# Kernel tuning notes

Measured on AMD Instinct MI355X. Metric: run time of the kernel, lower is better.

Reference implementation:

```python
import jax, jax.numpy as jnp
import numpy as np
from jax import lax

B, N, T, H, E, D, K = 2, 1024, 4096, 256, 2, 2, 9


def angle2vector(a):
    return jnp.stack([jnp.sin(a), jnp.cos(a)], axis=-1)


def setup_inputs() -> dict:
    key = jax.random.key(0)
    ks = jax.random.split(key, 16)
    s = jnp.float32(0.05)
    return {
        "x": jax.random.normal(ks[0], (B, N, T), jnp.float32),
        "z": jax.random.uniform(ks[1], (B, T, E, D), jnp.float32, 0.0, 2.0 * np.pi),
        # encoder: depthwise conv (groups=N) then two 1x1 convs
        "dw_w": jax.random.normal(ks[2], (N, 1, K), jnp.float32) * s,
        "dw_b": jax.random.normal(ks[3], (N,), jnp.float32) * s,
        "w1": jax.random.normal(ks[4], (H, N), jnp.float32) * s,
        "b1": jax.random.normal(ks[5], (H,), jnp.float32) * s,
        "w2": jax.random.normal(ks[6], (H, H), jnp.float32) * s,
        "b2": jax.random.normal(ks[7], (H,), jnp.float32) * s,
        # heads (1x1 convs)
        "wm": jax.random.normal(ks[8], (E * D * 2, H), jnp.float32) * s,
        "bm": jax.random.normal(ks[9], (E * D * 2,), jnp.float32) * s,
        "wv": jax.random.normal(ks[10], (E * D, H), jnp.float32) * s,
        "bv": jax.random.normal(ks[11], (E * D,), jnp.float32) * s,
        # feature basis / readout params
        "receptive_fields": jax.random.uniform(ks[12], (N, E, D), jnp.float32, 0.0, 2.0 * np.pi),
        "ensemble_weights": jax.random.normal(ks[13], (N, E), jnp.float32),
        "final_scale": jax.random.normal(ks[14], (N,), jnp.float32) * s,
        "log_tuning_width": jnp.full((1,), np.log(2.0), jnp.float32),
    }


def reference(x, z, dw_w, dw_b, w1, b1, w2, b2, wm, bm, wv, bv,
              receptive_fields, ensemble_weights, final_scale, log_tuning_width):
    # ---- encoder ----
    # depthwise conv1d, kernel_size=K, padding='same', groups=N
    h = lax.conv_general_dilated(
        x, dw_w, window_strides=(1,), padding="SAME",
        feature_group_count=N, dimension_numbers=("NCH", "OIH", "NCH"))
    h = h + dw_b[None, :, None]
    h = jax.nn.relu(jnp.einsum("hn,bnt->bht", w1, h) + b1[None, :, None])
    h = jax.nn.relu(jnp.einsum("gh,bht->bgt", w2, h) + b2[None, :, None])

    # ---- heads ----
    mu = jnp.einsum("oh,bht->bot", wm, h) + bm[None, :, None]  # [B, E*D*2, T]
    mu = mu.transpose(0, 2, 1).reshape(B, T, E, D, 2)
    logvar = jnp.einsum("oh,bht->bot", wv, h) + bv[None, :, None]  # [B, E*D, T]
    logvar = logvar.transpose(0, 2, 1).reshape(B, T, E, D)
    # normalize encodings onto unit circle
    mu = mu / jnp.sqrt(jnp.sum(mu ** 2, axis=-1, keepdims=True))

    # ---- feature basis ('bump') ----
    zv = angle2vector(z)                     # [B, T, E, D, 2]
    rfv = angle2vector(receptive_fields)     # [N, E, D, 2]
    diff = zv[:, :, None] - rfv[None, None]  # [B, T, N, E, D, 2]
    dist = jnp.sum(diff ** 2, axis=(4, 5))   # [B, T, N, E]
    response = jnp.exp(-dist / jnp.exp(log_tuning_width))  # nonlinearity='exp'

    # ---- ensemble-weighted readout ----
    ew = jax.nn.softmax(ensemble_weights, axis=1)  # [N, E]
    responses = jnp.einsum("btne,ne->btn", response, ew)
    responses = responses * jnp.exp(final_scale)[None, None]
    responses = responses.transpose(0, 2, 1)  # [B, N, T]
    return responses, z, mu, logvar
```

## Files before the change

kernel.cpp:

```cpp
#include <hip/hip_runtime.h>
#include <hip/hip_bf16.h>

#define B_ 2
#define N_ 1024
#define T_ 4096
#define H_ 256
#define ROWS_ 8192

typedef float f32x4 __attribute__((ext_vector_type(4)));
typedef __bf16 bf16x8 __attribute__((ext_vector_type(8)));

__device__ __forceinline__ void gl16(const void* g, void* l) {
  __builtin_amdgcn_global_load_lds(
      (const __attribute__((address_space(1))) void*)g,
      (__attribute__((address_space(3))) void*)l, 16, 0, 0);
}

__global__ __launch_bounds__(256) void cvt_split(
    const float* __restrict__ w1, const float* __restrict__ w2,
    __bf16* __restrict__ w1h, __bf16* __restrict__ w1l,
    __bf16* __restrict__ w2h, __bf16* __restrict__ w2l) {
  int i = blockIdx.x * 256 + threadIdx.x;
  if (i < 262144) {
    float v = w1[i];
    __bf16 h = (__bf16)v;
    w1h[i] = h;
    w1l[i] = (__bf16)(v - (float)h);
  } else {
    int j = i - 262144;
    float v = w2[j];
    __bf16 h = (__bf16)v;
    w2h[j] = h;
    w2l[j] = (__bf16)(v - (float)h);
  }
}

__global__ __launch_bounds__(256) void dwconv_t(
    const float* __restrict__ x, const float* __restrict__ w,
    const float* __restrict__ bias, __bf16* __restrict__ h0h,
    __bf16* __restrict__ h0l) {
  __shared__ float xs[64][73];
  const int tid = threadIdx.x;
  const int t0 = blockIdx.x * 64;
  const int n0 = blockIdx.y * 64;
  const int b = blockIdx.z;
  for (int i = tid; i < 64 * 72; i += 256) {
    int rr = i / 72, cc = i % 72;
    int tt = t0 - 4 + cc;
    xs[rr][cc] = (tt >= 0 && tt < T_) ? x[((size_t)(b * N_ + n0 + rr)) * T_ + tt] : 0.f;
  }
  __syncthreads();
  const int nl = tid & 63;
  const int tg = tid >> 6;
  float wr[9];
  #pragma unroll
  for (int k = 0; k < 9; ++k) wr[k] = w[(n0 + nl) * 9 + k];
  const float bb = bias[n0 + nl];
  for (int j = 0; j < 16; ++j) {
    int tl = tg * 16 + j;
    float acc = bb;
    #pragma unroll
    for (int k = 0; k < 9; ++k) acc = fmaf(xs[nl][tl + k], wr[k], acc);
    size_t o = ((size_t)b * T_ + t0 + tl) * N_ + n0 + nl;
    __bf16 h = (__bf16)acc;
    h0h[o] = h;
    h0l[o] = (__bf16)(acc - (float)h);
  }
}

__global__ __launch_bounds__(256) void gemm3p(
    const __bf16* __restrict__ Ah, const __bf16* __restrict__ Al,
    const __bf16* __restrict__ Wh, const __bf16* __restrict__ Wl,
    const float* __restrict__ bias, __bf16* __restrict__ Oh,
    __bf16* __restrict__ Ol, int K, int relu) {
  __shared__ __bf16 As[2][2][128 * 32];
  __shared__ __bf16 Ws[2][2][64 * 32];
  const int tid = threadIdx.x;
  int orig = blockIdx.y * 4 + blockIdx.x;
  int rm = (orig & 7) * 32 + (orig >> 3);
  const int g0 = (rm & 3) * 64;
  const int row0 = (rm >> 2) * 128;

  const int sr = tid >> 2;
  const int sl = tid & 3;
  const size_t a_off0 = (size_t)(row0 + sr) * K + sl * 8;
  const size_t a_off1 = (size_t)(row0 + 64 + sr) * K + sl * 8;
  const size_t w_off = (size_t)(g0 + sr) * K + sl * 8;

  const int lane = tid & 63;
  const int wid = tid >> 6;
  const int wrr = (wid >> 1) * 64;
  const int wcc = (wid & 1) * 32;
  const int lr = lane & 15;
  const int ls = lane >> 4;

  f32x4 acc[4][2];
  #pragma unroll
  for (int i = 0; i < 4; ++i)
    #pragma unroll
    for (int j = 0; j < 2; ++j) acc[i][j] = (f32x4)0.f;

  auto STAGE = [&](int buf, int k0) {
    gl16(Ah + a_off0 + k0, &As[buf][0][tid * 8]);
    gl16(Ah + a_off1 + k0, &As[buf][0][(tid + 256) * 8]);
    gl16(Al + a_off0 + k0, &As[buf][1][tid * 8]);
    gl16(Al + a_off1 + k0, &As[buf][1][(tid + 256) * 8]);
    gl16(Wh + w_off + k0, &Ws[buf][0][tid * 8]);
    gl16(Wl + w_off + k0, &Ws[buf][1][tid * 8]);
  };

  const int nk = K >> 5;
  STAGE(0, 0);
  __syncthreads();
  for (int kt = 0; kt < nk; ++kt) {
    const int cur = kt & 1;
    if (kt + 1 < nk) STAGE(cur ^ 1, (kt + 1) << 5);
    bf16x8 ah[4], al[4], wh[2], wl[2];
    #pragma unroll
    for (int mi = 0; mi < 4; ++mi) {
      int r = wrr + mi * 16 + lr;
      ah[mi] = *(const bf16x8*)&As[cur][0][r * 32 + ls * 8];
      al[mi] = *(const bf16x8*)&As[cur][1][r * 32 + ls * 8];
    }
    #pragma unroll
    for (int ni = 0; ni < 2; ++ni) {
      int r = wcc + ni * 16 + lr;
      wh[ni] = *(const bf16x8*)&Ws[cur][0][r * 32 + ls * 8];
      wl[ni] = *(const bf16x8*)&Ws[cur][1][r * 32 + ls * 8];
    }
    #pragma unroll
    for (int mi = 0; mi < 4; ++mi)
      #pragma unroll
      for (int ni = 0; ni < 2; ++ni) {
        acc[mi][ni] = __builtin_amdgcn_mfma_f32_16x16x32_bf16(ah[mi], wh[ni], acc[mi][ni], 0, 0, 0);
        acc[mi][ni] = __builtin_amdgcn_mfma_f32_16x16x32_bf16(ah[mi], wl[ni], acc[mi][ni], 0, 0, 0);
        acc[mi][ni] = __builtin_amdgcn_mfma_f32_16x16x32_bf16(al[mi], wh[ni], acc[mi][ni], 0, 0, 0);
      }
    __syncthreads();
  }

  #pragma unroll
  for (int ni = 0; ni < 2; ++ni) {
    const int g = g0 + wcc + ni * 16 + lr;
    const float bb = bias[g];
    #pragma unroll
    for (int mi = 0; mi < 4; ++mi)
      #pragma unroll
      for (int reg = 0; reg < 4; ++reg) {
        int t = row0 + wrr + mi * 16 + ls * 4 + reg;
        float v = acc[mi][ni][reg] + bb;
        if (relu) v = fmaxf(v, 0.f);
        __bf16 h = (__bf16)v;
        Oh[(size_t)t * H_ + g] = h;
        Ol[(size_t)t * H_ + g] = (__bf16)(v - (float)h);
      }
  }
}

__global__ __launch_bounds__(256) void heads_t(
    const __bf16* __restrict__ h2h, const __bf16* __restrict__ h2l,
    const float* __restrict__ wm, const float* __restrict__ bm,
    const float* __restrict__ wv, const float* __restrict__ bv,
    float* __restrict__ out_mu, float* __restrict__ out_lv) {
  __shared__ float sw[12][256];
  const int tid = threadIdx.x;
  for (int i = tid; i < 8 * 256; i += 256) sw[i >> 8][i & 255] = wm[i];
  for (int i = tid; i < 4 * 256; i += 256) sw[8 + (i >> 8)][i & 255] = wv[i];
  __syncthreads();
  const int tq = tid & 3;
  const int tl = tid >> 2;
  const size_t row = blockIdx.x * 64 + tl;
  float s[12];
  #pragma unroll
  for (int o = 0; o < 12; ++o) s[o] = 0.f;
  for (int j = 0; j < 8; ++j) {
    int jj = (j + tq * 2) & 7;
    int k0 = tq * 64 + jj * 8;
    bf16x8 vh = *(const bf16x8*)&h2h[row * 256 + k0];
    bf16x8 vl = *(const bf16x8*)&h2l[row * 256 + k0];
    #pragma unroll
    for (int e = 0; e < 8; ++e) {
      float v = (float)vh[e] + (float)vl[e];
      #pragma unroll
      for (int o = 0; o < 12; ++o) s[o] = fmaf(sw[o][k0 + e], v, s[o]);
    }
  }
  #pragma unroll
  for (int o = 0; o < 12; ++o) {
    s[o] += __shfl_xor(s[o], 1);
    s[o] += __shfl_xor(s[o], 2);
  }
  if (tq == 0) {
    float4 m01, m23;
    float mm[8];
    #pragma unroll
    for (int ed = 0; ed < 4; ++ed) {
      float m0 = s[ed * 2] + bm[ed * 2];
      float m1 = s[ed * 2 + 1] + bm[ed * 2 + 1];
      float inv = 1.f / sqrtf(m0 * m0 + m1 * m1);
      mm[ed * 2] = m0 * inv;
      mm[ed * 2 + 1] = m1 * inv;
    }
    m01 = make_float4(mm[0], mm[1], mm[2], mm[3]);
    m23 = make_float4(mm[4], mm[5], mm[6], mm[7]);
    *(float4*)&out_mu[row * 8] = m01;
    *(float4*)&out_mu[row * 8 + 4] = m23;
  } else if (tq == 1) {
    float4 lv = make_float4(s[8] + bv[0], s[9] + bv[1], s[10] + bv[2], s[11] + bv[3]);
    *(float4*)&out_lv[row * 4] = lv;
  }
}

__global__ __launch_bounds__(256) void resp_kernel(
    const float* __restrict__ z, const float* __restrict__ rf,
    const float* __restrict__ ew, const float* __restrict__ fs,
    const float* __restrict__ ltw, float* __restrict__ out,
    float* __restrict__ out_z) {
  __shared__ float s_sin[64][4];
  __shared__ float s_cos[64][4];
  __shared__ float s_w[64][2];
  const int tid = threadIdx.x;
  const int tc = blockIdx.x;
  const int nc = blockIdx.y;
  const int b = blockIdx.z;
  {
    int nl = tid >> 2, ed = tid & 3;
    float a = rf[(nc * 64 + nl) * 4 + ed];
    s_sin[nl][ed] = sinf(a);
    s_cos[nl][ed] = cosf(a);
  }
  if (tid < 64) {
    int n = nc * 64 + tid;
    float e0 = ew[n * 2], e1 = ew[n * 2 + 1];
    float m = fmaxf(e0, e1);
    float x0 = expf(e0 - m), x1 = expf(e1 - m);
    float sc = expf(fs[n]) / (x0 + x1);
    s_w[tid][0] = x0 * sc;
    s_w[tid][1] = x1 * sc;
  }
  __syncthreads();
  const int t = tc * 256 + tid;
  const float inv_tw = expf(-ltw[0]);
  float4 zv = *(const float4*)&z[((size_t)b * T_ + t) * 4];
  if (nc == 0) *(float4*)&out_z[((size_t)b * T_ + t) * 4] = zv;
  float sz0 = sinf(zv.x), cz0 = cosf(zv.x);
  float sz1 = sinf(zv.y), cz1 = cosf(zv.y);
  float sz2 = sinf(zv.z), cz2 = cosf(zv.z);
  float sz3 = sinf(zv.w), cz3 = cosf(zv.w);
  float* op = out + (size_t)b * N_ * T_ + (size_t)(nc * 64) * T_ + t;
  #pragma unroll 4
  for (int nl = 0; nl < 64; ++nl) {
    float dot0 = sz0 * s_sin[nl][0] + cz0 * s_cos[nl][0] +
                 sz1 * s_sin[nl][1] + cz1 * s_cos[nl][1];
    float dot1 = sz2 * s_sin[nl][2] + cz2 * s_cos[nl][2] +
                 sz3 * s_sin[nl][3] + cz3 * s_cos[nl][3];
    float r0 = __expf((2.f * dot0 - 4.f) * inv_tw);
    float r1 = __expf((2.f * dot1 - 4.f) * inv_tw);
    op[(size_t)nl * T_] = s_w[nl][0] * r0 + s_w[nl][1] * r1;
  }
}

extern "C" void kernel_launch(void* const* d_in, const int* in_sizes, int n_in,
                              void* d_out, int out_size, void* d_ws, size_t ws_size,
                              hipStream_t stream) {
  const float* x   = (const float*)d_in[0];
  const float* z   = (const float*)d_in[1];
  const float* dww = (const float*)d_in[2];
  const float* dwb = (const float*)d_in[3];
  const float* w1  = (const float*)d_in[4];
  const float* b1  = (const float*)d_in[5];
  const float* w2  = (const float*)d_in[6];
  const float* b2  = (const float*)d_in[7];
  const float* wm  = (const float*)d_in[8];
  const float* bm  = (const float*)d_in[9];
  const float* wv  = (const float*)d_in[10];
  const float* bv  = (const float*)d_in[11];
  const float* rf  = (const float*)d_in[12];
  const float* ew  = (const float*)d_in[13];
  const float* fs  = (const float*)d_in[14];
  const float* ltw = (const float*)d_in[15];

  float* out = (float*)d_out;
  float* out_resp = out;
  float* out_z    = out + (size_t)B_ * N_ * T_;
  float* out_mu   = out_z + (size_t)B_ * T_ * 4;
  float* out_lv   = out_mu + (size_t)B_ * T_ * 8;

  __bf16* h0h = (__bf16*)out_resp;
  __bf16* h0l = h0h + (size_t)ROWS_ * N_;

  __bf16* p = (__bf16*)d_ws;
  __bf16* w1h = p; p += 262144;
  __bf16* w1l = p; p += 262144;
  __bf16* w2h = p; p += 65536;
  __bf16* w2l = p; p += 65536;
  __bf16* h1h = p; p += (size_t)ROWS_ * H_;
  __bf16* h1l = p; p += (size_t)ROWS_ * H_;
  __bf16* h2h = p; p += (size_t)ROWS_ * H_;
  __bf16* h2l = p; p += (size_t)ROWS_ * H_;

  cvt_split<<<1280, 256, 0, stream>>>(w1, w2, w1h, w1l, w2h, w2l);
  dwconv_t<<<dim3(T_ / 64, N_ / 64, B_), 256, 0, stream>>>(x, dww, dwb, h0h, h0l);
  gemm3p<<<dim3(4, ROWS_ / 128, 1), 256, 0, stream>>>(
      h0h, h0l, w1h, w1l, b1, h1h, h1l, N_, 1);
  gemm3p<<<dim3(4, ROWS_ / 128, 1), 256, 0, stream>>>(
      h1h, h1l, w2h, w2l, b2, h2h, h2l, H_, 1);
  heads_t<<<dim3(ROWS_ / 64), 256, 0, stream>>>(
      h2h, h2l, wm, bm, wv, bv, out_mu, out_lv);
  resp_kernel<<<dim3(T_ / 256, N_ / 64, B_), 256, 0, stream>>>(
      z, rf, ew, fs, ltw, out_resp, out_z);
}
```

Before: 197.3 us.

## Shrink GEMM row tile to 64, swizzle LDS, and register-window the dwconv

```diff
diff --git a/kernel.cpp b/kernel.cpp
--- a/kernel.cpp
+++ b/kernel.cpp
@@ -39,7 +39,7 @@
     const float* __restrict__ x, const float* __restrict__ w,
     const float* __restrict__ bias, __bf16* __restrict__ h0h,
     __bf16* __restrict__ h0l) {
-  __shared__ float xs[64][73];
+  __shared__ float xs[64][76];
   const int tid = threadIdx.x;
   const int t0 = blockIdx.x * 64;
   const int n0 = blockIdx.y * 64;
@@ -49,22 +49,26 @@
     int tt = t0 - 4 + cc;
     xs[rr][cc] = (tt >= 0 && tt < T_) ? x[((size_t)(b * N_ + n0 + rr)) * T_ + tt] : 0.f;
   }
-  __syncthreads();
   const int nl = tid & 63;
   const int tg = tid >> 6;
   float wr[9];
   #pragma unroll
   for (int k = 0; k < 9; ++k) wr[k] = w[(n0 + nl) * 9 + k];
   const float bb = bias[n0 + nl];
+  __syncthreads();
+  float win[24];
+  #pragma unroll
+  for (int c = 0; c < 6; ++c)
+    *(f32x4*)&win[c * 4] = *(const f32x4*)&xs[nl][tg * 16 + c * 4];
+  const size_t obase = ((size_t)b * T_ + t0 + tg * 16) * N_ + n0 + nl;
+  #pragma unroll
   for (int j = 0; j < 16; ++j) {
-    int tl = tg * 16 + j;
     float acc = bb;
     #pragma unroll
-    for (int k = 0; k < 9; ++k) acc = fmaf(xs[nl][tl + k], wr[k], acc);
-    size_t o = ((size_t)b * T_ + t0 + tl) * N_ + n0 + nl;
+    for (int k = 0; k < 9; ++k) acc = fmaf(win[j + k], wr[k], acc);
     __bf16 h = (__bf16)acc;
-    h0h[o] = h;
-    h0l[o] = (__bf16)(acc - (float)h);
+    h0h[obase + (size_t)j * N_] = h;
+    h0l[obase + (size_t)j * N_] = (__bf16)(acc - (float)h);
   }
 }
 
@@ -73,41 +77,41 @@
     const __bf16* __restrict__ Wh, const __bf16* __restrict__ Wl,
     const float* __restrict__ bias, __bf16* __restrict__ Oh,
     __bf16* __restrict__ Ol, int K, int relu) {
-  __shared__ __bf16 As[2][2][128 * 32];
+  __shared__ __bf16 As[2][2][64 * 32];
   __shared__ __bf16 Ws[2][2][64 * 32];
   const int tid = threadIdx.x;
-  int orig = blockIdx.y * 4 + blockIdx.x;
-  int rm = (orig & 7) * 32 + (orig >> 3);
+  const int orig = blockIdx.x;
+  const int rm = (orig & 7) * 64 + (orig >> 3);
   const int g0 = (rm & 3) * 64;
-  const int row0 = (rm >> 2) * 128;
+  const int row0 = (rm >> 2) * 64;
 
   const int sr = tid >> 2;
   const int sl = tid & 3;
-  const size_t a_off0 = (size_t)(row0 + sr) * K + sl * 8;
-  const size_t a_off1 = (size_t)(row0 + 64 + sr) * K + sl * 8;
-  const size_t w_off = (size_t)(g0 + sr) * K + sl * 8;
+  const int ssl = sl ^ ((sr >> 1) & 3);
+  const size_t a_off = (size_t)(row0 + sr) * K + ssl * 8;
+  const size_t w_off = (size_t)(g0 + sr) * K + ssl * 8;
 
   const int lane = tid & 63;
   const int wid = tid >> 6;
-  const int wrr = (wid >> 1) * 64;
+  const int wrr = (wid >> 1) * 32;
   const int wcc = (wid & 1) * 32;
   const int lr = lane & 15;
   const int ls = lane >> 4;
 
-  f32x4 acc[4][2];
-  #pragma unroll
-  for (int i = 0; i < 4; ++i)
+  f32x4 acc[2][2];
+  #pragma unroll
+  for (int i = 0; i < 2; ++i)
     #pragma unroll
     for (int j = 0; j < 2; ++j) acc[i][j] = (f32x4)0.f;
 
   auto STAGE = [&](int buf, int k0) {
-    gl16(Ah + a_off0 + k0, &As[buf][0][tid * 8]);
-    gl16(Ah + a_off1 + k0, &As[buf][0][(tid + 256) * 8]);
-    gl16(Al + a_off0 + k0, &As[buf][1][tid * 8]);
-    gl16(Al + a_off1 + k0, &As[buf][1][(tid + 256) * 8]);
+    gl16(Ah + a_off + k0, &As[buf][0][tid * 8]);
+    gl16(Al + a_off + k0, &As[buf][1][tid * 8]);
     gl16(Wh + w_off + k0, &Ws[buf][0][tid * 8]);
     gl16(Wl + w_off + k0, &Ws[buf][1][tid * 8]);
   };
+
+  auto FADDR = [&](int r) { return r * 32 + (ls ^ ((r >> 1) & 3)) * 8; };
 
   const int nk = K >> 5;
   STAGE(0, 0);
@@ -115,21 +119,21 @@
   for (int kt = 0; kt < nk; ++kt) {
     const int cur = kt & 1;
     if (kt + 1 < nk) STAGE(cur ^ 1, (kt + 1) << 5);
-    bf16x8 ah[4], al[4], wh[2], wl[2];
-    #pragma unroll
-    for (int mi = 0; mi < 4; ++mi) {
-      int r = wrr + mi * 16 + lr;
-      ah[mi] = *(const bf16x8*)&As[cur][0][r * 32 + ls * 8];
-      al[mi] = *(const bf16x8*)&As[cur][1][r * 32 + ls * 8];
+    bf16x8 ah[2], al[2], wh[2], wl[2];
+    #pragma unroll
+    for (int mi = 0; mi < 2; ++mi) {
+      int a = FADDR(wrr + mi * 16 + lr);
+      ah[mi] = *(const bf16x8*)&As[cur][0][a];
+      al[mi] = *(const bf16x8*)&As[cur][1][a];
     }
     #pragma unroll
     for (int ni = 0; ni < 2; ++ni) {
-      int r = wcc + ni * 16 + lr;
-      wh[ni] = *(const bf16x8*)&Ws[cur][0][r * 32 + ls * 8];
-      wl[ni] = *(const bf16x8*)&Ws[cur][1][r * 32 + ls * 8];
+      int a = FADDR(wcc + ni * 16 + lr);
+      wh[ni] = *(const bf16x8*)&Ws[cur][0][a];
+      wl[ni] = *(const bf16x8*)&Ws[cur][1][a];
     }
     #pragma unroll
-    for (int mi = 0; mi < 4; ++mi)
+    for (int mi = 0; mi < 2; ++mi)
       #pragma unroll
       for (int ni = 0; ni < 2; ++ni) {
         acc[mi][ni] = __builtin_amdgcn_mfma_f32_16x16x32_bf16(ah[mi], wh[ni], acc[mi][ni], 0, 0, 0);
@@ -144,7 +148,7 @@
     const int g = g0 + wcc + ni * 16 + lr;
     const float bb = bias[g];
     #pragma unroll
-    for (int mi = 0; mi < 4; ++mi)
+    for (int mi = 0; mi < 2; ++mi)
       #pragma unroll
       for (int reg = 0; reg < 4; ++reg) {
         int t = row0 + wrr + mi * 16 + ls * 4 + reg;
@@ -191,7 +195,6 @@
     s[o] += __shfl_xor(s[o], 2);
   }
   if (tq == 0) {
-    float4 m01, m23;
     float mm[8];
     #pragma unroll
     for (int ed = 0; ed < 4; ++ed) {
@@ -201,13 +204,11 @@
       mm[ed * 2] = m0 * inv;
       mm[ed * 2 + 1] = m1 * inv;
     }
-    m01 = make_float4(mm[0], mm[1], mm[2], mm[3]);
-    m23 = make_float4(mm[4], mm[5], mm[6], mm[7]);
-    *(float4*)&out_mu[row * 8] = m01;
-    *(float4*)&out_mu[row * 8 + 4] = m23;
+    *(float4*)&out_mu[row * 8] = make_float4(mm[0], mm[1], mm[2], mm[3]);
+    *(float4*)&out_mu[row * 8 + 4] = make_float4(mm[4], mm[5], mm[6], mm[7]);
   } else if (tq == 1) {
-    float4 lv = make_float4(s[8] + bv[0], s[9] + bv[1], s[10] + bv[2], s[11] + bv[3]);
-    *(float4*)&out_lv[row * 4] = lv;
+    *(float4*)&out_lv[row * 4] =
+        make_float4(s[8] + bv[0], s[9] + bv[1], s[10] + bv[2], s[11] + bv[3]);
   }
 }
 
@@ -301,10 +302,8 @@
 
   cvt_split<<<1280, 256, 0, stream>>>(w1, w2, w1h, w1l, w2h, w2l);
   dwconv_t<<<dim3(T_ / 64, N_ / 64, B_), 256, 0, stream>>>(x, dww, dwb, h0h, h0l);
-  gemm3p<<<dim3(4, ROWS_ / 128, 1), 256, 0, stream>>>(
-      h0h, h0l, w1h, w1l, b1, h1h, h1l, N_, 1);
-  gemm3p<<<dim3(4, ROWS_ / 128, 1), 256, 0, stream>>>(
-      h1h, h1l, w2h, w2l, b2, h2h, h2l, H_, 1);
+  gemm3p<<<dim3(512), 256, 0, stream>>>(h0h, h0l, w1h, w1l, b1, h1h, h1l, N_, 1);
+  gemm3p<<<dim3(512), 256, 0, stream>>>(h1h, h1l, w2h, w2l, b2, h2h, h2l, H_, 1);
   heads_t<<<dim3(ROWS_ / 64), 256, 0, stream>>>(
       h2h, h2l, wm, bm, wv, bv, out_mu, out_lv);
   resp_kernel<<<dim3(T_ / 256, N_ / 64, B_), 256, 0, stream>>>(
```

Measured after the change: 183.0 us. 7.2% less time.
